# Kernel tuning notes

Hardware: AMD Instinct MI355X
Metric: run time of the kernel (lower is better)

## Reference

```python
import jax, jax.numpy as jnp
import numpy as np

B, Q, D, C, N = 4, 100, 128, 20, 262144
LN_EPS = 1e-5


def setup_inputs() -> dict:
    key = jax.random.key(0)
    ks = jax.random.split(key, 8)
    s = 1.0 / np.sqrt(D).astype(np.float32)
    return {
        "query_feat": jax.random.normal(ks[0], (B, Q, D), jnp.float32),
        "point_feats": jax.random.normal(ks[1], (N, D), jnp.float32),
        "batch_ids": jnp.sort(jax.random.randint(ks[2], (N,), 0, B, dtype=jnp.int32)),
        "ln_gamma": jnp.ones((D,), jnp.float32),
        "ln_beta": jnp.zeros((D,), jnp.float32),
        "W1": jax.random.normal(ks[3], (D, D), jnp.float32) * s,
        "b1": jnp.zeros((D,), jnp.float32),
        "W2": jax.random.normal(ks[4], (D, D), jnp.float32) * s,
        "b2": jnp.zeros((D,), jnp.float32),
        "Wc": jax.random.normal(ks[5], (C, D), jnp.float32) * s,
        "bc": jnp.zeros((C,), jnp.float32),
    }


def reference(query_feat, point_feats, batch_ids, ln_gamma, ln_beta, W1, b1, W2, b2, Wc, bc):
    # decoder_norm: LayerNorm over hidden dim
    mu = jnp.mean(query_feat, axis=-1, keepdims=True)
    var = jnp.var(query_feat, axis=-1, keepdims=True)
    qn = (query_feat - mu) * jax.lax.rsqrt(var + LN_EPS) * ln_gamma + ln_beta  # [B,Q,D]

    # mask_embed_head: Linear -> ReLU -> Linear (torch Linear: x @ W.T + b)
    h = jax.nn.relu(jnp.einsum('bqd,ed->bqe', qn, W1) + b1)
    mask_embed = jnp.einsum('bqd,ed->bqe', h, W2) + b2  # [B,Q,D]

    # class_embed_head
    outputs_class = jnp.einsum('bqd,cd->bqc', qn, Wc) + bc  # [B,Q,C]

    # Ragged per-batch matmul: for each point n, point_feats[n] @ mask_embed[batch_ids[n]].T.
    # Equivalent to the original concat of decomposed_features[i] @ mask_embed[i].T
    # because batch_ids is sorted. Loop is over the small fixed batch count only.
    nb = mask_embed.shape[0]
    out_masks = jnp.zeros((point_feats.shape[0], mask_embed.shape[1]), point_feats.dtype)
    for b in range(nb):
        sel = (batch_ids == b)[:, None]
        out_masks = out_masks + jnp.where(sel, point_feats @ mask_embed[b].T, 0.0)
    return outputs_class, out_masks
```

## Files before the change

kernel.cpp:

```cpp
#include <hip/hip_runtime.h>
#include <hip/hip_bf16.h>

typedef __bf16 bf16x8 __attribute__((ext_vector_type(8)));
typedef float f32x4 __attribute__((ext_vector_type(4)));
typedef unsigned short ushort8 __attribute__((ext_vector_type(8)));

#define B_    4
#define Q_    100
#define QPAD  112
#define D_    128
#define C_    20
#define N_    262144
#define TN    256
#define CPB   2
#define LROW  136
#define LN_EPS 1e-5f

__global__ __launch_bounds__(128) void head_kernel(
    const float* __restrict__ qf,
    const float* __restrict__ gamma, const float* __restrict__ beta,
    const float* __restrict__ W1, const float* __restrict__ b1,
    const float* __restrict__ W2, const float* __restrict__ b2,
    const float* __restrict__ Wc, const float* __restrict__ bc,
    float* __restrict__ out_class,
    unsigned short* __restrict__ me_hi, unsigned short* __restrict__ me_lo)
{
    const int q = blockIdx.x;
    const int b = blockIdx.y;
    const int t = threadIdx.x;

    unsigned short* mh = me_hi + (b * QPAD + q) * D_;
    unsigned short* ml = me_lo + (b * QPAD + q) * D_;
    if (q >= Q_) { mh[t] = 0; ml[t] = 0; return; }

    __shared__ float red[D_];
    __shared__ float qs[D_];
    __shared__ float hs[D_];

    const float x = qf[(b * Q_ + q) * D_ + t];

    red[t] = x;
    __syncthreads();
    #pragma unroll
    for (int s = 64; s > 0; s >>= 1) { if (t < s) red[t] += red[t + s]; __syncthreads(); }
    const float mu = red[0] * (1.0f / 128.0f);
    __syncthreads();
    const float xc = x - mu;
    red[t] = xc * xc;
    __syncthreads();
    #pragma unroll
    for (int s = 64; s > 0; s >>= 1) { if (t < s) red[t] += red[t + s]; __syncthreads(); }
    const float var = red[0] * (1.0f / 128.0f);

    const float xn = xc * rsqrtf(var + LN_EPS) * gamma[t] + beta[t];
    qs[t] = xn;
    __syncthreads();

    {
        const float4* wr = (const float4*)(W1 + t * D_);
        float p0 = 0.f, p1 = 0.f, p2 = 0.f, p3 = 0.f;
        #pragma unroll
        for (int d4 = 0; d4 < 32; ++d4) {
            const float4 w = wr[d4];
            const int d = d4 * 4;
            p0 = fmaf(w.x, qs[d + 0], p0);
            p1 = fmaf(w.y, qs[d + 1], p1);
            p2 = fmaf(w.z, qs[d + 2], p2);
            p3 = fmaf(w.w, qs[d + 3], p3);
        }
        hs[t] = fmaxf((p0 + p1) + (p2 + p3) + b1[t], 0.0f);
    }
    __syncthreads();

    {
        const float4* wr = (const float4*)(W2 + t * D_);
        float p0 = 0.f, p1 = 0.f, p2 = 0.f, p3 = 0.f;
        #pragma unroll
        for (int d4 = 0; d4 < 32; ++d4) {
            const float4 w = wr[d4];
            const int d = d4 * 4;
            p0 = fmaf(w.x, hs[d + 0], p0);
            p1 = fmaf(w.y, hs[d + 1], p1);
            p2 = fmaf(w.z, hs[d + 2], p2);
            p3 = fmaf(w.w, hs[d + 3], p3);
        }
        const float me = (p0 + p1) + (p2 + p3) + b2[t];
        const __bf16 hi = (__bf16)me;
        const __bf16 lo = (__bf16)(me - (float)hi);
        mh[t] = __builtin_bit_cast(unsigned short, hi);
        ml[t] = __builtin_bit_cast(unsigned short, lo);
    }

    if (t < C_) {
        const float4* wr = (const float4*)(Wc + t * D_);
        float p0 = 0.f, p1 = 0.f, p2 = 0.f, p3 = 0.f;
        #pragma unroll
        for (int d4 = 0; d4 < 32; ++d4) {
            const float4 w = wr[d4];
            const int d = d4 * 4;
            p0 = fmaf(w.x, qs[d + 0], p0);
            p1 = fmaf(w.y, qs[d + 1], p1);
            p2 = fmaf(w.z, qs[d + 2], p2);
            p3 = fmaf(w.w, qs[d + 3], p3);
        }
        out_class[(b * Q_ + q) * C_ + t] = (p0 + p1) + (p2 + p3) + bc[t];
    }
}

__global__ __launch_bounds__(1024, 4) void mask_kernel(
    const float* __restrict__ points, const int* __restrict__ bids,
    const unsigned short* __restrict__ me_hi, const unsigned short* __restrict__ me_lo,
    float* __restrict__ outm)
{
    const int tid  = threadIdx.x;
    const int wave = tid >> 6;
    const int lane = tid & 63;
    const int ar   = lane & 15;
    const int kg   = lane >> 4;
    const int qlane = lane & 15;

    __shared__ unsigned short BH[QPAD][LROW];
    __shared__ unsigned short BL[QPAD][LROW];

    int staged_b = -1;
    const int base = blockIdx.x * (TN * CPB);

    float4 fv[8];
    {
        const float* prow = points + (size_t)(base + wave * 16 + ar) * D_;
        #pragma unroll
        for (int kt = 0; kt < 4; ++kt) {
            fv[2 * kt]     = *(const float4*)(prow + kt * 32 + kg * 8);
            fv[2 * kt + 1] = *(const float4*)(prow + kt * 32 + kg * 8 + 4);
        }
    }

    for (int k = 0; k < CPB; ++k) {
        const int n0 = base + k * TN;

        bf16x8 AH[4], AL[4];
        #pragma unroll
        for (int kt = 0; kt < 4; ++kt) {
            const float f0[4] = {fv[2*kt].x, fv[2*kt].y, fv[2*kt].z, fv[2*kt].w};
            const float f1[4] = {fv[2*kt+1].x, fv[2*kt+1].y, fv[2*kt+1].z, fv[2*kt+1].w};
            #pragma unroll
            for (int j = 0; j < 4; ++j) {
                const __bf16 h0 = (__bf16)f0[j];
                AH[kt][j] = h0;
                AL[kt][j] = (__bf16)(f0[j] - (float)h0);
                const __bf16 h1 = (__bf16)f1[j];
                AH[kt][j + 4] = h1;
                AL[kt][j + 4] = (__bf16)(f1[j] - (float)h1);
            }
        }

        if (k + 1 < CPB) {
            const float* prow = points + (size_t)(n0 + TN + wave * 16 + ar) * D_;
            #pragma unroll
            for (int kt = 0; kt < 4; ++kt) {
                fv[2 * kt]     = *(const float4*)(prow + kt * 32 + kg * 8);
                fv[2 * kt + 1] = *(const float4*)(prow + kt * 32 + kg * 8 + 4);
            }
        }

        int  myb[4];
        long nout[4];
        #pragma unroll
        for (int rr = 0; rr < 4; ++rr) {
            const int row = n0 + wave * 16 + kg * 4 + rr;
            myb[rr]  = bids[row];
            nout[rr] = (long)row * Q_;
        }

        const int b_lo = bids[n0];
        const int b_hi = bids[n0 + TN - 1];

        for (int b = b_lo; b <= b_hi; ++b) {
            if (b != staged_b) {
                __syncthreads();
                const ushort8* sh = (const ushort8*)(me_hi + (size_t)b * QPAD * D_);
                const ushort8* sl = (const ushort8*)(me_lo + (size_t)b * QPAD * D_);
                for (int c = tid; c < QPAD * D_ / 8; c += 1024) {
                    const int row = c >> 4;
                    const int col = c & 15;
                    *(ushort8*)&BH[row][col * 8] = sh[c];
                    *(ushort8*)&BL[row][col * 8] = sl[c];
                }
                __syncthreads();
                staged_b = b;
            }

            #pragma unroll
            for (int qt = 0; qt < 7; ++qt) {
                f32x4 acc = {0.f, 0.f, 0.f, 0.f};
                const int qrow = qt * 16 + qlane;
                #pragma unroll
                for (int kt = 0; kt < 4; ++kt) {
                    const int kb = kt * 32 + kg * 8;
                    const bf16x8 bh = __builtin_bit_cast(bf16x8, *(const ushort8*)&BH[qrow][kb]);
                    const bf16x8 bl = __builtin_bit_cast(bf16x8, *(const ushort8*)&BL[qrow][kb]);
                    acc = __builtin_amdgcn_mfma_f32_16x16x32_bf16(AL[kt], bh, acc, 0, 0, 0);
                    acc = __builtin_amdgcn_mfma_f32_16x16x32_bf16(AH[kt], bl, acc, 0, 0, 0);
                    acc = __builtin_amdgcn_mfma_f32_16x16x32_bf16(AH[kt], bh, acc, 0, 0, 0);
                }
                if (qrow < Q_) {
                    #pragma unroll
                    for (int rr = 0; rr < 4; ++rr) {
                        if (myb[rr] == b) outm[nout[rr] + qrow] = acc[rr];
                    }
                }
            }
        }
    }
}

extern "C" void kernel_launch(void* const* d_in, const int* in_sizes, int n_in,
                              void* d_out, int out_size, void* d_ws, size_t ws_size,
                              hipStream_t stream) {
    const float* qf    = (const float*)d_in[0];
    const float* pf    = (const float*)d_in[1];
    const int*   bids  = (const int*)  d_in[2];
    const float* gamma = (const float*)d_in[3];
    const float* beta  = (const float*)d_in[4];
    const float* W1    = (const float*)d_in[5];
    const float* b1    = (const float*)d_in[6];
    const float* W2    = (const float*)d_in[7];
    const float* b2    = (const float*)d_in[8];
    const float* Wc    = (const float*)d_in[9];
    const float* bc    = (const float*)d_in[10];

    float* out_class = (float*)d_out;
    float* out_masks = out_class + B_ * Q_ * C_;

    unsigned short* me_hi = (unsigned short*)d_ws;
    unsigned short* me_lo = me_hi + B_ * QPAD * D_;

    head_kernel<<<dim3(QPAD, B_), 128, 0, stream>>>(
        qf, gamma, beta, W1, b1, W2, b2, Wc, bc, out_class, me_hi, me_lo);

    mask_kernel<<<dim3(N_ / (TN * CPB)), 1024, 0, stream>>>(
        pf, bids, me_hi, me_lo, out_masks);
}
```

Baseline: 282.4 us.

## Give each wave four row strips so B-fragment LDS reads are reused

The mask kernel now launches 256-thread blocks over 256 points, and each wave handles 64 rows (four 16-row strips) instead of 16. The hi/lo mask-embed fragments are read from LDS once per q-tile and reused across the four strips, which cuts LDS traffic per MFMA. Batch ids are packed into a single register and point loads are double-buffered during conversion. In exchange, each thread holds more registers (16 A-fragment pairs), and the smaller blocks stage the embed tile into LDS more often, lowering occupancy per block.

```diff
diff --git a/kernel.cpp b/kernel.cpp
--- a/kernel.cpp
+++ b/kernel.cpp
@@ -12,7 +12,6 @@
 #define C_    20
 #define N_    262144
 #define TN    256
-#define CPB   2
 #define LROW  136
 #define LN_EPS 1e-5f
 
@@ -107,106 +106,114 @@
     }
 }
 
-__global__ __launch_bounds__(1024, 4) void mask_kernel(
+__device__ __forceinline__ void load_strip(const float* __restrict__ prow,
+                                           float4 fv[8], int kg)
+{
+    #pragma unroll
+    for (int kt = 0; kt < 4; ++kt) {
+        fv[2 * kt]     = *(const float4*)(prow + kt * 32 + kg * 8);
+        fv[2 * kt + 1] = *(const float4*)(prow + kt * 32 + kg * 8 + 4);
+    }
+}
+
+__device__ __forceinline__ void conv_strip(const float4 fv[8],
+                                           bf16x8 AH[4], bf16x8 AL[4])
+{
+    #pragma unroll
+    for (int kt = 0; kt < 4; ++kt) {
+        const float f0[4] = {fv[2*kt].x, fv[2*kt].y, fv[2*kt].z, fv[2*kt].w};
+        const float f1[4] = {fv[2*kt+1].x, fv[2*kt+1].y, fv[2*kt+1].z, fv[2*kt+1].w};
+        #pragma unroll
+        for (int j = 0; j < 4; ++j) {
+            const __bf16 h0 = (__bf16)f0[j];
+            AH[kt][j] = h0;
+            AL[kt][j] = (__bf16)(f0[j] - (float)h0);
+            const __bf16 h1 = (__bf16)f1[j];
+            AH[kt][j + 4] = h1;
+            AL[kt][j + 4] = (__bf16)(f1[j] - (float)h1);
+        }
+    }
+}
+
+__global__ __launch_bounds__(256, 2) void mask_kernel(
     const float* __restrict__ points, const int* __restrict__ bids,
     const unsigned short* __restrict__ me_hi, const unsigned short* __restrict__ me_lo,
     float* __restrict__ outm)
 {
+    const int n0   = blockIdx.x * TN;
     const int tid  = threadIdx.x;
     const int wave = tid >> 6;
     const int lane = tid & 63;
     const int ar   = lane & 15;
     const int kg   = lane >> 4;
     const int qlane = lane & 15;
+    const int r0   = n0 + wave * 64;
 
     __shared__ unsigned short BH[QPAD][LROW];
     __shared__ unsigned short BL[QPAD][LROW];
 
-    int staged_b = -1;
-    const int base = blockIdx.x * (TN * CPB);
-
-    float4 fv[8];
-    {
-        const float* prow = points + (size_t)(base + wave * 16 + ar) * D_;
-        #pragma unroll
-        for (int kt = 0; kt < 4; ++kt) {
-            fv[2 * kt]     = *(const float4*)(prow + kt * 32 + kg * 8);
-            fv[2 * kt + 1] = *(const float4*)(prow + kt * 32 + kg * 8 + 4);
-        }
-    }
-
-    for (int k = 0; k < CPB; ++k) {
-        const int n0 = base + k * TN;
-
-        bf16x8 AH[4], AL[4];
-        #pragma unroll
-        for (int kt = 0; kt < 4; ++kt) {
-            const float f0[4] = {fv[2*kt].x, fv[2*kt].y, fv[2*kt].z, fv[2*kt].w};
-            const float f1[4] = {fv[2*kt+1].x, fv[2*kt+1].y, fv[2*kt+1].z, fv[2*kt+1].w};
-            #pragma unroll
-            for (int j = 0; j < 4; ++j) {
-                const __bf16 h0 = (__bf16)f0[j];
-                AH[kt][j] = h0;
-                AL[kt][j] = (__bf16)(f0[j] - (float)h0);
-                const __bf16 h1 = (__bf16)f1[j];
-                AH[kt][j + 4] = h1;
-                AL[kt][j + 4] = (__bf16)(f1[j] - (float)h1);
+    float4 fva[8], fvb[8];
+    load_strip(points + (size_t)(r0 + 0 * 16 + ar) * D_, fva, kg);
+    load_strip(points + (size_t)(r0 + 1 * 16 + ar) * D_, fvb, kg);
+
+    unsigned int pk = 0;
+    #pragma unroll
+    for (int s = 0; s < 4; ++s) {
+        #pragma unroll
+        for (int rr = 0; rr < 4; ++rr) {
+            pk |= (unsigned)bids[r0 + s * 16 + kg * 4 + rr] << ((s * 4 + rr) * 2);
+        }
+    }
+    const int b_lo = bids[n0];
+    const int b_hi = bids[n0 + TN - 1];
+
+    bf16x8 AH[4][4], AL[4][4];
+    conv_strip(fva, AH[0], AL[0]);
+    load_strip(points + (size_t)(r0 + 2 * 16 + ar) * D_, fva, kg);
+    conv_strip(fvb, AH[1], AL[1]);
+    load_strip(points + (size_t)(r0 + 3 * 16 + ar) * D_, fvb, kg);
+    conv_strip(fva, AH[2], AL[2]);
+    conv_strip(fvb, AH[3], AL[3]);
+
+    for (int b = b_lo; b <= b_hi; ++b) {
+        if (b != b_lo) __syncthreads();
+        {
+            const ushort8* sh = (const ushort8*)(me_hi + (size_t)b * QPAD * D_);
+            const ushort8* sl = (const ushort8*)(me_lo + (size_t)b * QPAD * D_);
+            for (int c = tid; c < QPAD * D_ / 8; c += 256) {
+                const int row = c >> 4;
+                const int col = c & 15;
+                *(ushort8*)&BH[row][col * 8] = sh[c];
+                *(ushort8*)&BL[row][col * 8] = sl[c];
             }
         }
-
-        if (k + 1 < CPB) {
-            const float* prow = points + (size_t)(n0 + TN + wave * 16 + ar) * D_;
+        __syncthreads();
+
+        #pragma unroll
+        for (int qt = 0; qt < 7; ++qt) {
+            const int qrow = qt * 16 + qlane;
+            bf16x8 bh[4], bl[4];
             #pragma unroll
             for (int kt = 0; kt < 4; ++kt) {
-                fv[2 * kt]     = *(const float4*)(prow + kt * 32 + kg * 8);
-                fv[2 * kt + 1] = *(const float4*)(prow + kt * 32 + kg * 8 + 4);
+                const int kb = kt * 32 + kg * 8;
+                bh[kt] = __builtin_bit_cast(bf16x8, *(const ushort8*)&BH[qrow][kb]);
+                bl[kt] = __builtin_bit_cast(bf16x8, *(const ushort8*)&BL[qrow][kb]);
             }
-        }
-
-        int  myb[4];
-        long nout[4];
-        #pragma unroll
-        for (int rr = 0; rr < 4; ++rr) {
-            const int row = n0 + wave * 16 + kg * 4 + rr;
-            myb[rr]  = bids[row];
-            nout[rr] = (long)row * Q_;
-        }
-
-        const int b_lo = bids[n0];
-        const int b_hi = bids[n0 + TN - 1];
-
-        for (int b = b_lo; b <= b_hi; ++b) {
-            if (b != staged_b) {
-                __syncthreads();
-                const ushort8* sh = (const ushort8*)(me_hi + (size_t)b * QPAD * D_);
-                const ushort8* sl = (const ushort8*)(me_lo + (size_t)b * QPAD * D_);
-                for (int c = tid; c < QPAD * D_ / 8; c += 1024) {
-                    const int row = c >> 4;
-                    const int col = c & 15;
-                    *(ushort8*)&BH[row][col * 8] = sh[c];
-                    *(ushort8*)&BL[row][col * 8] = sl[c];
-                }
-                __syncthreads();
-                staged_b = b;
-            }
-
             #pragma unroll
-            for (int qt = 0; qt < 7; ++qt) {
+            for (int s = 0; s < 4; ++s) {
                 f32x4 acc = {0.f, 0.f, 0.f, 0.f};
-                const int qrow = qt * 16 + qlane;
                 #pragma unroll
                 for (int kt = 0; kt < 4; ++kt) {
-                    const int kb = kt * 32 + kg * 8;
-                    const bf16x8 bh = __builtin_bit_cast(bf16x8, *(const ushort8*)&BH[qrow][kb]);
-                    const bf16x8 bl = __builtin_bit_cast(bf16x8, *(const ushort8*)&BL[qrow][kb]);
-                    acc = __builtin_amdgcn_mfma_f32_16x16x32_bf16(AL[kt], bh, acc, 0, 0, 0);
-                    acc = __builtin_amdgcn_mfma_f32_16x16x32_bf16(AH[kt], bl, acc, 0, 0, 0);
-                    acc = __builtin_amdgcn_mfma_f32_16x16x32_bf16(AH[kt], bh, acc, 0, 0, 0);
+                    acc = __builtin_amdgcn_mfma_f32_16x16x32_bf16(AL[s][kt], bh[kt], acc, 0, 0, 0);
+                    acc = __builtin_amdgcn_mfma_f32_16x16x32_bf16(AH[s][kt], bl[kt], acc, 0, 0, 0);
+                    acc = __builtin_amdgcn_mfma_f32_16x16x32_bf16(AH[s][kt], bh[kt], acc, 0, 0, 0);
                 }
                 if (qrow < Q_) {
                     #pragma unroll
                     for (int rr = 0; rr < 4; ++rr) {
-                        if (myb[rr] == b) outm[nout[rr] + qrow] = acc[rr];
+                        if (((pk >> ((s * 4 + rr) * 2)) & 3u) == (unsigned)b) {
+                            outm[(size_t)(r0 + s * 16 + kg * 4 + rr) * Q_ + qrow] = acc[rr];
+                        }
                     }
                 }
             }
@@ -238,6 +245,6 @@
     head_kernel<<<dim3(QPAD, B_), 128, 0, stream>>>(
         qf, gamma, beta, W1, b1, W2, b2, Wc, bc, out_class, me_hi, me_lo);
 
-    mask_kernel<<<dim3(N_ / (TN * CPB)), 1024, 0, stream>>>(
+    mask_kernel<<<dim3(N_ / TN), 256, 0, stream>>>(
         pf, bids, me_hi, me_lo, out_masks);
 }
```

Result: slower. 294.3 us (+4.2%).

## Restructure mask kernel: batch-outer loop with 512-thread blocks and 4 chunks

Applied to the files above, without the earlier changes.

The mask kernel now uses 512-thread blocks, each covering 4 chunks of 128 rows, and loops over batch ids outermost. The mask-embed tile is staged into LDS once per batch and all chunks are processed against it. This drops the per-chunk staging checks and replaces per-row batch-id loads with one vectorized int4 load. In exchange, a block whose span crosses a batch boundary reloads and recomputes every chunk for each batch present, redoing MFMA work on boundary blocks.

```diff
diff --git a/kernel.cpp b/kernel.cpp
--- a/kernel.cpp
+++ b/kernel.cpp
@@ -11,8 +11,9 @@
 #define D_    128
 #define C_    20
 #define N_    262144
-#define TN    256
-#define CPB   2
+#define RPC   128
+#define CPB   4
+#define SPAN  (RPC * CPB)
 #define LROW  136
 #define LN_EPS 1e-5f
 
@@ -107,7 +108,36 @@
     }
 }
 
-__global__ __launch_bounds__(1024, 4) void mask_kernel(
+__device__ __forceinline__ void load_strip(const float* __restrict__ prow,
+                                           float4 fv[8], int kg)
+{
+    #pragma unroll
+    for (int kt = 0; kt < 4; ++kt) {
+        fv[2 * kt]     = *(const float4*)(prow + kt * 32 + kg * 8);
+        fv[2 * kt + 1] = *(const float4*)(prow + kt * 32 + kg * 8 + 4);
+    }
+}
+
+__device__ __forceinline__ void conv_strip(const float4 fv[8],
+                                           bf16x8 AH[4], bf16x8 AL[4])
+{
+    #pragma unroll
+    for (int kt = 0; kt < 4; ++kt) {
+        const float f0[4] = {fv[2*kt].x, fv[2*kt].y, fv[2*kt].z, fv[2*kt].w};
+        const float f1[4] = {fv[2*kt+1].x, fv[2*kt+1].y, fv[2*kt+1].z, fv[2*kt+1].w};
+        #pragma unroll
+        for (int j = 0; j < 4; ++j) {
+            const __bf16 h0 = (__bf16)f0[j];
+            AH[kt][j] = h0;
+            AL[kt][j] = (__bf16)(f0[j] - (float)h0);
+            const __bf16 h1 = (__bf16)f1[j];
+            AH[kt][j + 4] = h1;
+            AL[kt][j + 4] = (__bf16)(f1[j] - (float)h1);
+        }
+    }
+}
+
+__global__ __launch_bounds__(512, 4) void mask_kernel(
     const float* __restrict__ points, const int* __restrict__ bids,
     const unsigned short* __restrict__ me_hi, const unsigned short* __restrict__ me_lo,
     float* __restrict__ outm)
@@ -118,82 +148,47 @@
     const int ar   = lane & 15;
     const int kg   = lane >> 4;
     const int qlane = lane & 15;
+    const int base = blockIdx.x * SPAN;
 
     __shared__ unsigned short BH[QPAD][LROW];
     __shared__ unsigned short BL[QPAD][LROW];
 
-    int staged_b = -1;
-    const int base = blockIdx.x * (TN * CPB);
-
-    float4 fv[8];
-    {
-        const float* prow = points + (size_t)(base + wave * 16 + ar) * D_;
-        #pragma unroll
-        for (int kt = 0; kt < 4; ++kt) {
-            fv[2 * kt]     = *(const float4*)(prow + kt * 32 + kg * 8);
-            fv[2 * kt + 1] = *(const float4*)(prow + kt * 32 + kg * 8 + 4);
-        }
-    }
-
-    for (int k = 0; k < CPB; ++k) {
-        const int n0 = base + k * TN;
-
-        bf16x8 AH[4], AL[4];
-        #pragma unroll
-        for (int kt = 0; kt < 4; ++kt) {
-            const float f0[4] = {fv[2*kt].x, fv[2*kt].y, fv[2*kt].z, fv[2*kt].w};
-            const float f1[4] = {fv[2*kt+1].x, fv[2*kt+1].y, fv[2*kt+1].z, fv[2*kt+1].w};
-            #pragma unroll
-            for (int j = 0; j < 4; ++j) {
-                const __bf16 h0 = (__bf16)f0[j];
-                AH[kt][j] = h0;
-                AL[kt][j] = (__bf16)(f0[j] - (float)h0);
-                const __bf16 h1 = (__bf16)f1[j];
-                AH[kt][j + 4] = h1;
-                AL[kt][j + 4] = (__bf16)(f1[j] - (float)h1);
+    const int b_lo = bids[base];
+    const int b_hi = bids[base + SPAN - 1];
+
+    for (int b = b_lo; b <= b_hi; ++b) {
+        if (b != b_lo) __syncthreads();
+        {
+            const ushort8* sh = (const ushort8*)(me_hi + (size_t)b * QPAD * D_);
+            const ushort8* sl = (const ushort8*)(me_lo + (size_t)b * QPAD * D_);
+            for (int c = tid; c < QPAD * D_ / 8; c += 512) {
+                const int row = c >> 4;
+                const int col = c & 15;
+                *(ushort8*)&BH[row][col * 8] = sh[c];
+                *(ushort8*)&BL[row][col * 8] = sl[c];
             }
         }
-
-        if (k + 1 < CPB) {
-            const float* prow = points + (size_t)(n0 + TN + wave * 16 + ar) * D_;
-            #pragma unroll
-            for (int kt = 0; kt < 4; ++kt) {
-                fv[2 * kt]     = *(const float4*)(prow + kt * 32 + kg * 8);
-                fv[2 * kt + 1] = *(const float4*)(prow + kt * 32 + kg * 8 + 4);
-            }
-        }
-
-        int  myb[4];
-        long nout[4];
-        #pragma unroll
-        for (int rr = 0; rr < 4; ++rr) {
-            const int row = n0 + wave * 16 + kg * 4 + rr;
-            myb[rr]  = bids[row];
-            nout[rr] = (long)row * Q_;
-        }
-
-        const int b_lo = bids[n0];
-        const int b_hi = bids[n0 + TN - 1];
-
-        for (int b = b_lo; b <= b_hi; ++b) {
-            if (b != staged_b) {
-                __syncthreads();
-                const ushort8* sh = (const ushort8*)(me_hi + (size_t)b * QPAD * D_);
-                const ushort8* sl = (const ushort8*)(me_lo + (size_t)b * QPAD * D_);
-                for (int c = tid; c < QPAD * D_ / 8; c += 1024) {
-                    const int row = c >> 4;
-                    const int col = c & 15;
-                    *(ushort8*)&BH[row][col * 8] = sh[c];
-                    *(ushort8*)&BL[row][col * 8] = sl[c];
-                }
-                __syncthreads();
-                staged_b = b;
-            }
+        __syncthreads();
+
+        float4 fv[8];
+        load_strip(points + (size_t)(base + wave * 16 + ar) * D_, fv, kg);
+
+        for (int c = 0; c < CPB; ++c) {
+            const int row0 = base + c * RPC + wave * 16;
+
+            bf16x8 AH[4], AL[4];
+            conv_strip(fv, AH, AL);
+
+            if (c + 1 < CPB)
+                load_strip(points + (size_t)(row0 + RPC + ar) * D_, fv, kg);
+
+            const int4 mb = *(const int4*)(bids + row0 + kg * 4);
+            const int myb[4] = {mb.x, mb.y, mb.z, mb.w};
 
             #pragma unroll
             for (int qt = 0; qt < 7; ++qt) {
+                const int qrow = qt * 16 + qlane;
                 f32x4 acc = {0.f, 0.f, 0.f, 0.f};
-                const int qrow = qt * 16 + qlane;
                 #pragma unroll
                 for (int kt = 0; kt < 4; ++kt) {
                     const int kb = kt * 32 + kg * 8;
@@ -206,7 +201,8 @@
                 if (qrow < Q_) {
                     #pragma unroll
                     for (int rr = 0; rr < 4; ++rr) {
-                        if (myb[rr] == b) outm[nout[rr] + qrow] = acc[rr];
+                        if (myb[rr] == b)
+                            outm[(size_t)(row0 + kg * 4 + rr) * Q_ + qrow] = acc[rr];
                     }
                 }
             }
@@ -238,6 +234,6 @@
     head_kernel<<<dim3(QPAD, B_), 128, 0, stream>>>(
         qf, gamma, beta, W1, b1, W2, b2, Wc, bc, out_class, me_hi, me_lo);
 
-    mask_kernel<<<dim3(N_ / (TN * CPB)), 1024, 0, stream>>>(
+    mask_kernel<<<dim3(N_ / SPAN), 512, 0, stream>>>(
         pf, bids, me_hi, me_lo, out_masks);
 }
```

Result: slower. 565.8 us (+100.4%).
